# Kernel tuning notes

Hardware: AMD Instinct MI355X
Metric: run time of the kernel (lower is better)

## Reference

```python
import jax, jax.numpy as jnp
import numpy as np

DT = 0.1
DEATH_THRESHOLD = 0.05


def setup_inputs() -> dict:
    key = jax.random.key(0)
    ks = jax.random.split(key, 12)
    B, S, DE, DM, DC, DEPTH = 1, 4096, 256, 64, 64, 4
    DIN = DE + DC
    w_scale = 0.02  # keeps pre-softmax scores in a sane range
    return {
        "e": jax.random.normal(ks[0], (B, S, DE), jnp.float32),
        "E": jax.random.uniform(ks[1], (B, S, 1), jnp.float32),
        "P": jax.random.uniform(ks[2], (B, S, 1), jnp.float32),
        "G": jax.random.normal(ks[3], (B, S, 1), jnp.float32),
        "m": jax.random.uniform(ks[4], (B, S, DM), jnp.float32),
        "c": jax.random.normal(ks[5], (B, S, DC), jnp.float32),
        "l": jax.random.uniform(ks[6], (B, S, 1), jnp.float32),
        "wq": jax.random.normal(ks[7], (DEPTH, DIN, DE), jnp.float32) * w_scale,
        "bq": jnp.zeros((DEPTH, DE), jnp.float32),
        "wk": jax.random.normal(ks[8], (DEPTH, DIN, DE), jnp.float32) * w_scale,
        "bk": jnp.zeros((DEPTH, DE), jnp.float32),
        "wv": jax.random.normal(ks[9], (DEPTH, DIN, DE), jnp.float32) * w_scale,
        "bv": jnp.zeros((DEPTH, DE), jnp.float32),
        "alpha": jnp.full((DEPTH,), 1.0, jnp.float32),
        "beta": jnp.full((DEPTH,), 0.5, jnp.float32),
        "gamma": jnp.full((DEPTH,), 0.2, jnp.float32),
        "basal": jnp.full((DEPTH,), 0.05, jnp.float32),
    }


def reference(e, E, P, G, m, c, l, wq, bq, wk, bk, wv, bv, alpha, beta, gamma, basal):
    depth = wq.shape[0]
    scale = 1.0 / np.sqrt(wq.shape[-1]).astype(np.float32)
    for i in range(depth):
        # --- OuterTrans: multiplicatively-masked self-attention ---
        x = jnp.concatenate([e, c], axis=-1)                 # [B,S,DE+DC]
        q = x @ wq[i] + bq[i]
        k = x @ wk[i] + bk[i]
        v = x @ wv[i] + bv[i]
        scores = jnp.einsum("bsd,btd->bst", q, k) * scale    # [B,S,S]
        membrane = jnp.einsum("bsd,btd->bst", m, m)          # [B,S,S]
        lifespan = jnp.einsum("bsd,btd->bst", l, l)          # [B,S,S]
        attn = jax.nn.softmax(scores * membrane * lifespan, axis=-1)
        h_tilde = jnp.einsum("bst,btd->bsd", attn, v)        # [B,S,DE]
        e = e + h_tilde
        # --- ThermodynamicODE (elementwise per-token update) ---
        S_in = jnp.sum(h_tilde * h_tilde, axis=-1, keepdims=True)  # ||h||^2 [B,S,1]
        PE = P * E
        P_new = jax.nn.relu(P + (alpha[i] * S_in - beta[i] * PE) * DT)
        E_new = jax.nn.relu(E + (basal[i] - gamma[i] * PE) * DT)
        m_target = jax.nn.sigmoid(E_new - P_new)             # [B,S,1] broadcast to m
        G = G + (0.1 * E_new - 0.5 * P_new) * DT
        l_decay = 0.01 + 0.5 * jax.nn.relu(P_new - 2.0)
        m = 0.9 * m + 0.1 * m_target
        l = jnp.clip(l - l_decay * DT, 0.0, 1.0)
        E, P = E_new, P_new
    # Dynamic pruning: jit-compatible variant -> zero-mask dead cells instead of
    # data-dependent slicing; also return alive_mask and num_died.
    alive = l > DEATH_THRESHOLD                              # [B,S,1] bool
    af = alive.astype(e.dtype)
    num_died = e.shape[1] - jnp.sum(alive.astype(jnp.int32))
    return (e * af, E * af, P * af, G * af, m * af, c * af, l * af,
            alive[0, :, 0], num_died)
```

## Files before the change

kernel.cpp:

```cpp
#include <hip/hip_runtime.h>
#include <hip/hip_bf16.h>
#include <math.h>

#define SS 4096
#define DE 256
#define DM 64
#define DC 64
#define DIN 320
#define DEPTH 4
#define DT_C 0.1f
#define KSPLIT 8
#define BK 32
#define EXP_SHIFT 8.0f

typedef float f32x4_t __attribute__((ext_vector_type(4)));
typedef __bf16 bf16x8_t __attribute__((ext_vector_type(8)));

#define MFMA_BF16(A, B, C) __builtin_amdgcn_mfma_f32_16x16x32_bf16((A), (B), (C), 0, 0, 0)

#define OFF_E     (SS*DE)
#define OFF_P     (OFF_E + SS)
#define OFF_G     (OFF_P + SS)
#define OFF_M     (OFF_G + SS)
#define OFF_C     (OFF_M + SS*DM)
#define OFF_L     (OFF_C + SS*DM)
#define OFF_ALIVE (OFF_L + SS)
#define OFF_DIED  (OFF_ALIVE + SS)

#define WS_EWS   0
#define WS_MWS   (WS_EWS  + SS*DE)
#define WS_EE    (WS_MWS  + SS*DM)
#define WS_PP    (WS_EE   + SS)
#define WS_GG    (WS_PP   + SS)
#define WS_LL    (WS_GG   + SS)
#define WS_SIN   (WS_LL   + SS)
#define WS_LSUM  (WS_SIN  + SS)
#define WS_OACC  (WS_LSUM + SS)
#define WS_XB    (WS_OACC + SS*DE)
#define WS_QB    (WS_XB  + SS*DIN/2)
#define WS_KB    (WS_QB  + SS*DE/2)
#define WS_VTB   (WS_KB  + SS*DE/2)
#define WS_MB    (WS_VTB + SS*DE/2)
#define WS_WT    (WS_MB  + SS*DM/2)

#define KT_STR 264
#define VT_STR 56
#define MT_STR 72
#define PT_STR 40

__global__ __launch_bounds__(256) void transpose_w_kernel(
    const float* __restrict__ wq, const float* __restrict__ wk, const float* __restrict__ wv,
    __hip_bfloat16* __restrict__ wt)
{
    const int zd = blockIdx.z;
    const int z = zd >> 2;
    const float* src = (z == 0 ? wq : (z == 1 ? wk : wv)) + (size_t)(zd & 3) * DIN * DE;
    __shared__ float t[32][33];
    const int k0 = blockIdx.x * 32;
    const int n0 = blockIdx.y * 32;
    const int tr = threadIdx.x >> 5;
    const int tc = threadIdx.x & 31;
    #pragma unroll
    for (int p = 0; p < 4; ++p)
        t[p*8 + tr][tc] = src[(size_t)(k0 + p*8 + tr) * DE + n0 + tc];
    __syncthreads();
    #pragma unroll
    for (int p = 0; p < 4; ++p) {
        int n = n0 + p*8 + tr;
        int k = k0 + tc;
        wt[((size_t)zd * DE + n) * DIN + k] = __float2bfloat16(t[tc][p*8 + tr]);
    }
}

__global__ __launch_bounds__(256) void cast_m_kernel(
    const float* __restrict__ m_in, float* __restrict__ m_ws, __hip_bfloat16* __restrict__ mb)
{
    const int idx = blockIdx.x * 256 + threadIdx.x;
    const float v = m_in[idx];
    m_ws[idx] = v;
    mb[idx] = __float2bfloat16(v);
}

__global__ __launch_bounds__(256) void build_x_kernel(
    const float* __restrict__ e_ws, const float* __restrict__ c, __hip_bfloat16* __restrict__ xb)
{
    const int idx = blockIdx.x * 256 + threadIdx.x;
    const int row = idx / 80, q = idx % 80;
    float4 v;
    if (q < 64) v = *(const float4*)&e_ws[(size_t)row * DE + q * 4];
    else        v = *(const float4*)&c[(size_t)row * DC + (q - 64) * 4];
    __hip_bfloat16 o[4] = {__float2bfloat16(v.x), __float2bfloat16(v.y),
                           __float2bfloat16(v.z), __float2bfloat16(v.w)};
    *(uint2*)&xb[(size_t)row * DIN + q * 4] = *(uint2*)o;
}

__global__ __launch_bounds__(256) void zero_kernel(float* __restrict__ O_acc, float* __restrict__ Lsum)
{
    const int idx = blockIdx.x * 256 + threadIdx.x;
    *(float4*)&O_acc[(size_t)idx * 4] = make_float4(0.f, 0.f, 0.f, 0.f);
    if (idx < SS) Lsum[idx] = 0.f;
}

__global__ __launch_bounds__(256, 2) void proj_mfma_kernel(
    const __hip_bfloat16* __restrict__ xb, const __hip_bfloat16* __restrict__ wt,
    const float* __restrict__ bq, const float* __restrict__ bk, const float* __restrict__ bv,
    __hip_bfloat16* __restrict__ qb, __hip_bfloat16* __restrict__ kb, __hip_bfloat16* __restrict__ vtb,
    int layer)
{
    const int z = blockIdx.z;
    const int tid = threadIdx.x;
    const int w = tid >> 6, lane = tid & 63;
    const int m = lane & 15, quad = lane >> 4;
    const int row0 = blockIdx.x * 16;
    const __hip_bfloat16* wtz = wt + (size_t)(z * DEPTH + layer) * DE * DIN;
    const float* bias = (z == 0 ? bq : (z == 1 ? bk : bv)) + (size_t)layer * DE;

    bf16x8_t xa[10];
    #pragma unroll
    for (int kk = 0; kk < 10; ++kk)
        xa[kk] = *(const bf16x8_t*)&xb[(size_t)(row0 + m) * DIN + kk * 32 + quad * 8];

    f32x4_t acc[4];
    #pragma unroll
    for (int nt = 0; nt < 4; ++nt) acc[nt] = (f32x4_t){0.f, 0.f, 0.f, 0.f};

    #pragma unroll
    for (int kk = 0; kk < 10; ++kk) {
        #pragma unroll
        for (int nt = 0; nt < 4; ++nt) {
            const int ncol = w * 64 + nt * 16 + m;
            bf16x8_t bfrag = *(const bf16x8_t*)&wtz[(size_t)ncol * DIN + kk * 32 + quad * 8];
            acc[nt] = MFMA_BF16(xa[kk], bfrag, acc[nt]);
        }
    }
    #pragma unroll
    for (int nt = 0; nt < 4; ++nt) {
        const int col = w * 64 + nt * 16 + m;
        const float b = bias[col];
        #pragma unroll
        for (int r = 0; r < 4; ++r) {
            const int row = row0 + quad * 4 + r;
            const __hip_bfloat16 h = __float2bfloat16(acc[nt][r] + b);
            if (z == 0)      qb[(size_t)row * DE + col] = h;
            else if (z == 1) kb[(size_t)row * DE + col] = h;
            else             vtb[(size_t)col * SS + row] = h;
        }
    }
}

__global__ __launch_bounds__(256, 2) void attn_mfma_kernel(
    const __hip_bfloat16* __restrict__ qb, const __hip_bfloat16* __restrict__ kb,
    const __hip_bfloat16* __restrict__ vtb, const __hip_bfloat16* __restrict__ mb,
    const float* __restrict__ l_ws,
    float* __restrict__ O_acc, float* __restrict__ Lsum)
{
    __shared__ __align__(16) __hip_bfloat16 kt[32 * KT_STR];
    __shared__ __align__(16) __hip_bfloat16 vt[256 * VT_STR];
    __shared__ __align__(16) __hip_bfloat16 mt[32 * MT_STR];
    __shared__ __align__(16) __hip_bfloat16 pt[4 * 16 * PT_STR];
    __shared__ float lt[32];

    const int tid = threadIdx.x;
    const int w = tid >> 6, lane = tid & 63;
    const int n = lane & 15, quad = lane >> 4;
    const int row0 = blockIdx.x * 64 + w * 16;
    const int t_begin = blockIdx.y * (SS / KSPLIT);

    bf16x8_t qa[8];
    #pragma unroll
    for (int kk = 0; kk < 8; ++kk)
        qa[kk] = *(const bf16x8_t*)&qb[(size_t)(row0 + n) * DE + kk * 32 + quad * 8];
    bf16x8_t ma[2];
    #pragma unroll
    for (int kk = 0; kk < 2; ++kk)
        ma[kk] = *(const bf16x8_t*)&mb[(size_t)(row0 + n) * DM + kk * 32 + quad * 8];
    float lq[4];
    #pragma unroll
    for (int r = 0; r < 4; ++r) lq[r] = l_ws[row0 + quad * 4 + r] * 0.0625f;

    f32x4_t oacc[16];
    #pragma unroll
    for (int ct = 0; ct < 16; ++ct) oacc[ct] = (f32x4_t){0.f, 0.f, 0.f, 0.f};
    float plsum[4] = {0.f, 0.f, 0.f, 0.f};
    __hip_bfloat16* ptw = &pt[w * 16 * PT_STR];

    for (int t0 = t_begin; t0 < t_begin + SS / KSPLIT; t0 += BK) {
        __syncthreads();
        #pragma unroll
        for (int p = 0; p < 4; ++p) {
            const int idx = tid + p * 256;
            const int row = idx >> 5, g = idx & 31;
            *(float4*)&kt[row * KT_STR + g * 8] = *(const float4*)&kb[(size_t)(t0 + row) * DE + g * 8];
        }
        #pragma unroll
        for (int p = 0; p < 4; ++p) {
            const int idx = tid + p * 256;
            const int col = idx >> 2, seg = idx & 3;
            *(float4*)&vt[col * VT_STR + seg * 8] = *(const float4*)&vtb[(size_t)col * SS + t0 + seg * 8];
        }
        {
            const int row = tid >> 3, g = tid & 7;
            *(float4*)&mt[row * MT_STR + g * 8] = *(const float4*)&mb[(size_t)(t0 + row) * DM + g * 8];
        }
        if (tid < 32) lt[tid] = l_ws[t0 + tid];
        __syncthreads();

        f32x4_t sqk0 = (f32x4_t){0.f,0.f,0.f,0.f}, sqk1 = (f32x4_t){0.f,0.f,0.f,0.f};
        f32x4_t smm0 = (f32x4_t){0.f,0.f,0.f,0.f}, smm1 = (f32x4_t){0.f,0.f,0.f,0.f};
        #pragma unroll
        for (int kk = 0; kk < 8; ++kk) {
            bf16x8_t k0 = *(const bf16x8_t*)&kt[n * KT_STR + kk * 32 + quad * 8];
            bf16x8_t k1 = *(const bf16x8_t*)&kt[(n + 16) * KT_STR + kk * 32 + quad * 8];
            sqk0 = MFMA_BF16(qa[kk], k0, sqk0);
            sqk1 = MFMA_BF16(qa[kk], k1, sqk1);
        }
        #pragma unroll
        for (int kk = 0; kk < 2; ++kk) {
            bf16x8_t m0 = *(const bf16x8_t*)&mt[n * MT_STR + kk * 32 + quad * 8];
            bf16x8_t m1 = *(const bf16x8_t*)&mt[(n + 16) * MT_STR + kk * 32 + quad * 8];
            smm0 = MFMA_BF16(ma[kk], m0, smm0);
            smm1 = MFMA_BF16(ma[kk], m1, smm1);
        }
        const float lk0 = lt[n], lk1 = lt[n + 16];
        #pragma unroll
        for (int r = 0; r < 4; ++r) {
            const float x0 = sqk0[r] * lq[r] * lk0 * smm0[r];
            const float x1 = sqk1[r] * lq[r] * lk1 * smm1[r];
            const float p0 = __expf(x0 - EXP_SHIFT);
            const float p1 = __expf(x1 - EXP_SHIFT);
            plsum[r] += p0 + p1;
            ptw[(quad * 4 + r) * PT_STR + n]      = __float2bfloat16(p0);
            ptw[(quad * 4 + r) * PT_STR + 16 + n] = __float2bfloat16(p1);
        }
        const bf16x8_t pa = *(const bf16x8_t*)&ptw[n * PT_STR + quad * 8];
        #pragma unroll
        for (int ct = 0; ct < 16; ++ct) {
            bf16x8_t vb = *(const bf16x8_t*)&vt[(ct * 16 + n) * VT_STR + quad * 8];
            oacc[ct] = MFMA_BF16(pa, vb, oacc[ct]);
        }
    }

    #pragma unroll
    for (int r = 0; r < 4; ++r) {
        float s = plsum[r];
        s += __shfl_xor(s, 1); s += __shfl_xor(s, 2);
        s += __shfl_xor(s, 4); s += __shfl_xor(s, 8);
        plsum[r] = s;
    }
    if (n == 0) {
        #pragma unroll
        for (int r = 0; r < 4; ++r)
            atomicAdd(&Lsum[row0 + quad * 4 + r], plsum[r]);
    }
    #pragma unroll
    for (int ct = 0; ct < 16; ++ct) {
        #pragma unroll
        for (int r = 0; r < 4; ++r)
            atomicAdd(&O_acc[(size_t)(row0 + quad * 4 + r) * DE + ct * 16 + n], oacc[ct][r]);
    }
}

__global__ __launch_bounds__(256) void combine_kernel(
    const float* __restrict__ O_acc, const float* __restrict__ Lsum,
    float* __restrict__ e_ws, float* __restrict__ S_in)
{
    const int w = threadIdx.x >> 6, lane = threadIdx.x & 63;
    const int row = blockIdx.x * 4 + w;
    const float invL = 1.0f / Lsum[row];
    float4 o = *(const float4*)&O_acc[(size_t)row * DE + lane * 4];
    o.x *= invL; o.y *= invL; o.z *= invL; o.w *= invL;
    float4 ev = *(float4*)&e_ws[(size_t)row * DE + lane * 4];
    ev.x += o.x; ev.y += o.y; ev.z += o.z; ev.w += o.w;
    *(float4*)&e_ws[(size_t)row * DE + lane * 4] = ev;
    float ssq = o.x*o.x + o.y*o.y + o.z*o.z + o.w*o.w;
    #pragma unroll
    for (int mask = 1; mask < 64; mask <<= 1) ssq += __shfl_xor(ssq, mask);
    if (lane == 0) S_in[row] = ssq;
}

__global__ __launch_bounds__(256) void ode_kernel(
    const float* __restrict__ S_in,
    float* __restrict__ E_ws, float* __restrict__ P_ws, float* __restrict__ G_ws,
    float* __restrict__ m_ws, __hip_bfloat16* __restrict__ mb, float* __restrict__ l_ws,
    const float* __restrict__ alpha, const float* __restrict__ beta,
    const float* __restrict__ gamma_, const float* __restrict__ basal, int layer)
{
    const int w = threadIdx.x >> 6, lane = threadIdx.x & 63;
    const int row = blockIdx.x * 4 + w;
    const float a = alpha[layer], b = beta[layer], gm = gamma_[layer], bas = basal[layer];
    const float E = E_ws[row], P = P_ws[row];
    const float Sin = S_in[row];
    const float PE = P * E;
    const float Pn = fmaxf(0.f, P + (a * Sin - b * PE) * DT_C);
    const float En = fmaxf(0.f, E + (bas - gm * PE) * DT_C);
    const float mtg = 1.f / (1.f + __expf(-(En - Pn)));
    const size_t mi = (size_t)row * DM + lane;
    const float mv = 0.9f * m_ws[mi] + 0.1f * mtg;
    m_ws[mi] = mv;
    mb[mi] = __float2bfloat16(mv);
    if (lane == 0) {
        E_ws[row] = En;
        P_ws[row] = Pn;
        G_ws[row] = G_ws[row] + (0.1f * En - 0.5f * Pn) * DT_C;
        const float ldec = 0.01f + 0.5f * fmaxf(0.f, Pn - 2.0f);
        const float lv = l_ws[row] - ldec * DT_C;
        l_ws[row] = fminf(1.f, fmaxf(0.f, lv));
    }
}

__global__ __launch_bounds__(256) void finalize_kernel(
    const float* __restrict__ e_ws, const float* __restrict__ E_ws, const float* __restrict__ P_ws,
    const float* __restrict__ G_ws, const float* __restrict__ m_ws, const float* __restrict__ c,
    const float* __restrict__ l_ws, float* __restrict__ out)
{
    const int srow = blockIdx.x;
    const int tid = threadIdx.x;
    const float lv = l_ws[srow];
    const float af = (lv > 0.05f) ? 1.f : 0.f;
    out[(size_t)srow * DE + tid] = e_ws[(size_t)srow * DE + tid] * af;
    if (tid < DM) {
        out[OFF_M + (size_t)srow * DM + tid] = m_ws[(size_t)srow * DM + tid] * af;
        out[OFF_C + (size_t)srow * DM + tid] = c[(size_t)srow * DM + tid] * af;
    }
    if (tid == 0) {
        out[OFF_E + srow] = E_ws[srow] * af;
        out[OFF_P + srow] = P_ws[srow] * af;
        out[OFF_G + srow] = G_ws[srow] * af;
        out[OFF_L + srow] = lv * af;
        out[OFF_ALIVE + srow] = af;
    }
}

__global__ __launch_bounds__(256) void count_kernel(const float* __restrict__ l_ws, float* __restrict__ out)
{
    __shared__ float sdata[4];
    const int tid = threadIdx.x;
    int cnt = 0;
    for (int i = tid; i < SS; i += 256) cnt += (l_ws[i] > 0.05f) ? 1 : 0;
    float f = (float)cnt;
    #pragma unroll
    for (int mask = 1; mask < 64; mask <<= 1) f += __shfl_xor(f, mask);
    if ((tid & 63) == 0) sdata[tid >> 6] = f;
    __syncthreads();
    if (tid == 0) out[OFF_DIED] = (float)SS - (sdata[0] + sdata[1] + sdata[2] + sdata[3]);
}

extern "C" void kernel_launch(void* const* d_in, const int* in_sizes, int n_in,
                              void* d_out, int out_size, void* d_ws, size_t ws_size,
                              hipStream_t stream) {
    const float* e_in = (const float*)d_in[0];
    const float* E_in = (const float*)d_in[1];
    const float* P_in = (const float*)d_in[2];
    const float* G_in = (const float*)d_in[3];
    const float* m_in = (const float*)d_in[4];
    const float* c_in = (const float*)d_in[5];
    const float* l_in = (const float*)d_in[6];
    const float* wq = (const float*)d_in[7];
    const float* bq = (const float*)d_in[8];
    const float* wk = (const float*)d_in[9];
    const float* bk = (const float*)d_in[10];
    const float* wv = (const float*)d_in[11];
    const float* bv = (const float*)d_in[12];
    const float* alpha = (const float*)d_in[13];
    const float* beta  = (const float*)d_in[14];
    const float* gamma_ = (const float*)d_in[15];
    const float* basal = (const float*)d_in[16];
    float* out = (float*)d_out;
    float* ws = (float*)d_ws;

    float* e_ws = ws + WS_EWS;
    float* m_ws = ws + WS_MWS;
    float* E_ws = ws + WS_EE;
    float* P_ws = ws + WS_PP;
    float* G_ws = ws + WS_GG;
    float* l_ws = ws + WS_LL;
    float* S_in = ws + WS_SIN;
    float* Lsum = ws + WS_LSUM;
    float* O_acc = ws + WS_OACC;
    __hip_bfloat16* xb  = (__hip_bfloat16*)(ws + WS_XB);
    __hip_bfloat16* qb  = (__hip_bfloat16*)(ws + WS_QB);
    __hip_bfloat16* kb  = (__hip_bfloat16*)(ws + WS_KB);
    __hip_bfloat16* vtb = (__hip_bfloat16*)(ws + WS_VTB);
    __hip_bfloat16* mb  = (__hip_bfloat16*)(ws + WS_MB);
    __hip_bfloat16* wt  = (__hip_bfloat16*)(ws + WS_WT);

    hipMemcpyAsync(e_ws, e_in, (size_t)SS*DE*sizeof(float), hipMemcpyDeviceToDevice, stream);
    hipMemcpyAsync(E_ws, E_in, (size_t)SS*sizeof(float), hipMemcpyDeviceToDevice, stream);
    hipMemcpyAsync(P_ws, P_in, (size_t)SS*sizeof(float), hipMemcpyDeviceToDevice, stream);
    hipMemcpyAsync(G_ws, G_in, (size_t)SS*sizeof(float), hipMemcpyDeviceToDevice, stream);
    hipMemcpyAsync(l_ws, l_in, (size_t)SS*sizeof(float), hipMemcpyDeviceToDevice, stream);
    cast_m_kernel<<<dim3(SS*DM/256), 256, 0, stream>>>(m_in, m_ws, mb);
    transpose_w_kernel<<<dim3(DIN/32, DE/32, 12), 256, 0, stream>>>(wq, wk, wv, wt);

    for (int layer = 0; layer < DEPTH; ++layer) {
        zero_kernel<<<dim3(SS*DE/1024), 256, 0, stream>>>(O_acc, Lsum);
        build_x_kernel<<<dim3(SS*80/256), 256, 0, stream>>>(e_ws, c_in, xb);
        proj_mfma_kernel<<<dim3(SS/16, 1, 3), 256, 0, stream>>>(
            xb, wt, bq, bk, bv, qb, kb, vtb, layer);
        attn_mfma_kernel<<<dim3(SS/64, KSPLIT), 256, 0, stream>>>(
            qb, kb, vtb, mb, l_ws, O_acc, Lsum);
        combine_kernel<<<dim3(SS/4), 256, 0, stream>>>(O_acc, Lsum, e_ws, S_in);
        ode_kernel<<<dim3(SS/4), 256, 0, stream>>>(
            S_in, E_ws, P_ws, G_ws, m_ws, mb, l_ws, alpha, beta, gamma_, basal, layer);
    }
    finalize_kernel<<<dim3(SS), 256, 0, stream>>>(
        e_ws, E_ws, P_ws, G_ws, m_ws, c_in, l_ws, out);
    count_kernel<<<1, 256, 0, stream>>>(l_ws, out);
}
```

Before: 501.0 us.

## Fuse per-layer elementwise kernels, rebalance attention split, raise occupancy

Merges zero, build_x, combine and ode kernels into one fused combine kernel that also writes next-layer bf16 x and re-zeros accumulators, plus an init kernel replacing the e memcpy. Changes the key split from 8 to 12 with uneven tile ranges, raises attention launch bounds to 3 blocks/SM, shrinks V tile stride, and splits MFMA accumulation chains for more ILP. Aims to cut launch count and memory passes and improve attention occupancy, at risk of register spills from the tighter launch bound.

```diff
diff --git a/kernel.cpp b/kernel.cpp
--- a/kernel.cpp
+++ b/kernel.cpp
@@ -9,7 +9,7 @@
 #define DIN 320
 #define DEPTH 4
 #define DT_C 0.1f
-#define KSPLIT 8
+#define NSPLIT 12
 #define BK 32
 #define EXP_SHIFT 8.0f
 
@@ -44,7 +44,7 @@
 #define WS_WT    (WS_MB  + SS*DM/2)
 
 #define KT_STR 264
-#define VT_STR 56
+#define VT_STR 40
 #define MT_STR 72
 #define PT_STR 40
 
@@ -81,24 +81,19 @@
     mb[idx] = __float2bfloat16(v);
 }
 
-__global__ __launch_bounds__(256) void build_x_kernel(
-    const float* __restrict__ e_ws, const float* __restrict__ c, __hip_bfloat16* __restrict__ xb)
-{
-    const int idx = blockIdx.x * 256 + threadIdx.x;
-    const int row = idx / 80, q = idx % 80;
-    float4 v;
-    if (q < 64) v = *(const float4*)&e_ws[(size_t)row * DE + q * 4];
-    else        v = *(const float4*)&c[(size_t)row * DC + (q - 64) * 4];
-    __hip_bfloat16 o[4] = {__float2bfloat16(v.x), __float2bfloat16(v.y),
-                           __float2bfloat16(v.z), __float2bfloat16(v.w)};
-    *(uint2*)&xb[(size_t)row * DIN + q * 4] = *(uint2*)o;
-}
-
-__global__ __launch_bounds__(256) void zero_kernel(float* __restrict__ O_acc, float* __restrict__ Lsum)
-{
-    const int idx = blockIdx.x * 256 + threadIdx.x;
-    *(float4*)&O_acc[(size_t)idx * 4] = make_float4(0.f, 0.f, 0.f, 0.f);
-    if (idx < SS) Lsum[idx] = 0.f;
+__global__ __launch_bounds__(256) void init_kernel(
+    const float* __restrict__ e_in, const float* __restrict__ c_in,
+    float* __restrict__ e_ws, __hip_bfloat16* __restrict__ xb,
+    float* __restrict__ O_acc, float* __restrict__ Lsum)
+{
+    const int row = blockIdx.x;
+    const int tid = threadIdx.x;
+    const float v = e_in[(size_t)row * DE + tid];
+    e_ws[(size_t)row * DE + tid] = v;
+    xb[(size_t)row * DIN + tid] = __float2bfloat16(v);
+    O_acc[(size_t)row * DE + tid] = 0.f;
+    if (tid < DC) xb[(size_t)row * DIN + DE + tid] = __float2bfloat16(c_in[(size_t)row * DC + tid]);
+    if (tid == 0) Lsum[row] = 0.f;
 }
 
 __global__ __launch_bounds__(256, 2) void proj_mfma_kernel(
@@ -148,7 +143,7 @@
     }
 }
 
-__global__ __launch_bounds__(256, 2) void attn_mfma_kernel(
+__global__ __launch_bounds__(256, 3) void attn_mfma_kernel(
     const __hip_bfloat16* __restrict__ qb, const __hip_bfloat16* __restrict__ kb,
     const __hip_bfloat16* __restrict__ vtb, const __hip_bfloat16* __restrict__ mb,
     const float* __restrict__ l_ws,
@@ -164,7 +159,6 @@
     const int w = tid >> 6, lane = tid & 63;
     const int n = lane & 15, quad = lane >> 4;
     const int row0 = blockIdx.x * 64 + w * 16;
-    const int t_begin = blockIdx.y * (SS / KSPLIT);
 
     bf16x8_t qa[8];
     #pragma unroll
@@ -183,8 +177,13 @@
     for (int ct = 0; ct < 16; ++ct) oacc[ct] = (f32x4_t){0.f, 0.f, 0.f, 0.f};
     float plsum[4] = {0.f, 0.f, 0.f, 0.f};
     __hip_bfloat16* ptw = &pt[w * 16 * PT_STR];
-
-    for (int t0 = t_begin; t0 < t_begin + SS / KSPLIT; t0 += BK) {
+    const f32x4_t zf4 = (f32x4_t){0.f, 0.f, 0.f, 0.f};
+
+    const int it_begin = (blockIdx.y * 128) / NSPLIT;
+    const int it_end   = ((blockIdx.y + 1) * 128) / NSPLIT;
+
+    for (int it = it_begin; it < it_end; ++it) {
+        const int t0 = it * BK;
         __syncthreads();
         #pragma unroll
         for (int p = 0; p < 4; ++p) {
@@ -205,22 +204,38 @@
         if (tid < 32) lt[tid] = l_ws[t0 + tid];
         __syncthreads();
 
-        f32x4_t sqk0 = (f32x4_t){0.f,0.f,0.f,0.f}, sqk1 = (f32x4_t){0.f,0.f,0.f,0.f};
-        f32x4_t smm0 = (f32x4_t){0.f,0.f,0.f,0.f}, smm1 = (f32x4_t){0.f,0.f,0.f,0.f};
-        #pragma unroll
-        for (int kk = 0; kk < 8; ++kk) {
+        f32x4_t qk0 = zf4, qk1 = zf4, qk2 = zf4, qk3 = zf4;
+        #pragma unroll
+        for (int kk = 0; kk < 4; ++kk) {
             bf16x8_t k0 = *(const bf16x8_t*)&kt[n * KT_STR + kk * 32 + quad * 8];
             bf16x8_t k1 = *(const bf16x8_t*)&kt[(n + 16) * KT_STR + kk * 32 + quad * 8];
-            sqk0 = MFMA_BF16(qa[kk], k0, sqk0);
-            sqk1 = MFMA_BF16(qa[kk], k1, sqk1);
-        }
-        #pragma unroll
-        for (int kk = 0; kk < 2; ++kk) {
-            bf16x8_t m0 = *(const bf16x8_t*)&mt[n * MT_STR + kk * 32 + quad * 8];
-            bf16x8_t m1 = *(const bf16x8_t*)&mt[(n + 16) * MT_STR + kk * 32 + quad * 8];
-            smm0 = MFMA_BF16(ma[kk], m0, smm0);
-            smm1 = MFMA_BF16(ma[kk], m1, smm1);
-        }
+            qk0 = MFMA_BF16(qa[kk], k0, qk0);
+            qk2 = MFMA_BF16(qa[kk], k1, qk2);
+        }
+        #pragma unroll
+        for (int kk = 4; kk < 8; ++kk) {
+            bf16x8_t k0 = *(const bf16x8_t*)&kt[n * KT_STR + kk * 32 + quad * 8];
+            bf16x8_t k1 = *(const bf16x8_t*)&kt[(n + 16) * KT_STR + kk * 32 + quad * 8];
+            qk1 = MFMA_BF16(qa[kk], k0, qk1);
+            qk3 = MFMA_BF16(qa[kk], k1, qk3);
+        }
+        const f32x4_t sqk0 = qk0 + qk1;
+        const f32x4_t sqk1 = qk2 + qk3;
+
+        f32x4_t mm0a, mm0b, mm1a, mm1b;
+        {
+            bf16x8_t m00 = *(const bf16x8_t*)&mt[n * MT_STR + quad * 8];
+            bf16x8_t m01 = *(const bf16x8_t*)&mt[n * MT_STR + 32 + quad * 8];
+            bf16x8_t m10 = *(const bf16x8_t*)&mt[(n + 16) * MT_STR + quad * 8];
+            bf16x8_t m11 = *(const bf16x8_t*)&mt[(n + 16) * MT_STR + 32 + quad * 8];
+            mm0a = MFMA_BF16(ma[0], m00, zf4);
+            mm0b = MFMA_BF16(ma[1], m01, zf4);
+            mm1a = MFMA_BF16(ma[0], m10, zf4);
+            mm1b = MFMA_BF16(ma[1], m11, zf4);
+        }
+        const f32x4_t smm0 = mm0a + mm0b;
+        const f32x4_t smm1 = mm1a + mm1b;
+
         const float lk0 = lt[n], lk1 = lt[n + 16];
         #pragma unroll
         for (int r = 0; r < 4; ++r) {
@@ -260,9 +275,14 @@
     }
 }
 
-__global__ __launch_bounds__(256) void combine_kernel(
-    const float* __restrict__ O_acc, const float* __restrict__ Lsum,
-    float* __restrict__ e_ws, float* __restrict__ S_in)
+__global__ __launch_bounds__(256) void fused_combine_kernel(
+    float* __restrict__ O_acc, float* __restrict__ Lsum,
+    float* __restrict__ e_ws, __hip_bfloat16* __restrict__ xb,
+    float* __restrict__ S_in,
+    float* __restrict__ E_ws, float* __restrict__ P_ws, float* __restrict__ G_ws,
+    float* __restrict__ m_ws, __hip_bfloat16* __restrict__ mb, float* __restrict__ l_ws,
+    const float* __restrict__ alpha, const float* __restrict__ beta,
+    const float* __restrict__ gamma_, const float* __restrict__ basal, int layer)
 {
     const int w = threadIdx.x >> 6, lane = threadIdx.x & 63;
     const int row = blockIdx.x * 4 + w;
@@ -272,26 +292,22 @@
     float4 ev = *(float4*)&e_ws[(size_t)row * DE + lane * 4];
     ev.x += o.x; ev.y += o.y; ev.z += o.z; ev.w += o.w;
     *(float4*)&e_ws[(size_t)row * DE + lane * 4] = ev;
+    {
+        __hip_bfloat16 h4[4] = {__float2bfloat16(ev.x), __float2bfloat16(ev.y),
+                                __float2bfloat16(ev.z), __float2bfloat16(ev.w)};
+        *(uint2*)&xb[(size_t)row * DIN + lane * 4] = *(uint2*)h4;
+    }
+    *(float4*)&O_acc[(size_t)row * DE + lane * 4] = make_float4(0.f, 0.f, 0.f, 0.f);
+    if (lane == 0) Lsum[row] = 0.f;
+
     float ssq = o.x*o.x + o.y*o.y + o.z*o.z + o.w*o.w;
     #pragma unroll
     for (int mask = 1; mask < 64; mask <<= 1) ssq += __shfl_xor(ssq, mask);
-    if (lane == 0) S_in[row] = ssq;
-}
-
-__global__ __launch_bounds__(256) void ode_kernel(
-    const float* __restrict__ S_in,
-    float* __restrict__ E_ws, float* __restrict__ P_ws, float* __restrict__ G_ws,
-    float* __restrict__ m_ws, __hip_bfloat16* __restrict__ mb, float* __restrict__ l_ws,
-    const float* __restrict__ alpha, const float* __restrict__ beta,
-    const float* __restrict__ gamma_, const float* __restrict__ basal, int layer)
-{
-    const int w = threadIdx.x >> 6, lane = threadIdx.x & 63;
-    const int row = blockIdx.x * 4 + w;
+
     const float a = alpha[layer], b = beta[layer], gm = gamma_[layer], bas = basal[layer];
     const float E = E_ws[row], P = P_ws[row];
-    const float Sin = S_in[row];
     const float PE = P * E;
-    const float Pn = fmaxf(0.f, P + (a * Sin - b * PE) * DT_C);
+    const float Pn = fmaxf(0.f, P + (a * ssq - b * PE) * DT_C);
     const float En = fmaxf(0.f, E + (bas - gm * PE) * DT_C);
     const float mtg = 1.f / (1.f + __expf(-(En - Pn)));
     const size_t mi = (size_t)row * DM + lane;
@@ -299,6 +315,7 @@
     m_ws[mi] = mv;
     mb[mi] = __float2bfloat16(mv);
     if (lane == 0) {
+        S_in[row] = ssq;
         E_ws[row] = En;
         P_ws[row] = Pn;
         G_ws[row] = G_ws[row] + (0.1f * En - 0.5f * Pn) * DT_C;
@@ -384,24 +401,22 @@
     __hip_bfloat16* mb  = (__hip_bfloat16*)(ws + WS_MB);
     __hip_bfloat16* wt  = (__hip_bfloat16*)(ws + WS_WT);
 
-    hipMemcpyAsync(e_ws, e_in, (size_t)SS*DE*sizeof(float), hipMemcpyDeviceToDevice, stream);
     hipMemcpyAsync(E_ws, E_in, (size_t)SS*sizeof(float), hipMemcpyDeviceToDevice, stream);
     hipMemcpyAsync(P_ws, P_in, (size_t)SS*sizeof(float), hipMemcpyDeviceToDevice, stream);
     hipMemcpyAsync(G_ws, G_in, (size_t)SS*sizeof(float), hipMemcpyDeviceToDevice, stream);
     hipMemcpyAsync(l_ws, l_in, (size_t)SS*sizeof(float), hipMemcpyDeviceToDevice, stream);
     cast_m_kernel<<<dim3(SS*DM/256), 256, 0, stream>>>(m_in, m_ws, mb);
     transpose_w_kernel<<<dim3(DIN/32, DE/32, 12), 256, 0, stream>>>(wq, wk, wv, wt);
+    init_kernel<<<dim3(SS), 256, 0, stream>>>(e_in, c_in, e_ws, xb, O_acc, Lsum);
 
     for (int layer = 0; layer < DEPTH; ++layer) {
-        zero_kernel<<<dim3(SS*DE/1024), 256, 0, stream>>>(O_acc, Lsum);
-        build_x_kernel<<<dim3(SS*80/256), 256, 0, stream>>>(e_ws, c_in, xb);
         proj_mfma_kernel<<<dim3(SS/16, 1, 3), 256, 0, stream>>>(
             xb, wt, bq, bk, bv, qb, kb, vtb, layer);
-        attn_mfma_kernel<<<dim3(SS/64, KSPLIT), 256, 0, stream>>>(
+        attn_mfma_kernel<<<dim3(SS/64, NSPLIT), 256, 0, stream>>>(
             qb, kb, vtb, mb, l_ws, O_acc, Lsum);
-        combine_kernel<<<dim3(SS/4), 256, 0, stream>>>(O_acc, Lsum, e_ws, S_in);
-        ode_kernel<<<dim3(SS/4), 256, 0, stream>>>(
-            S_in, E_ws, P_ws, G_ws, m_ws, mb, l_ws, alpha, beta, gamma_, basal, layer);
+        fused_combine_kernel<<<dim3(SS/4), 256, 0, stream>>>(
+            O_acc, Lsum, e_ws, xb, S_in, E_ws, P_ws, G_ws, m_ws, mb, l_ws,
+            alpha, beta, gamma_, basal, layer);
     }
     finalize_kernel<<<dim3(SS), 256, 0, stream>>>(
         e_ws, E_ws, P_ws, G_ws, m_ws, c_in, l_ws, out);
```

New measurement: 550.1 us. 9.8% more time.
